# Optimization experiments

Measured on AMD Instinct MI355X. Metric: run time of the kernel, lower is better.

## Reference

```python
import jax, jax.numpy as jnp
import numpy as np

L, D, H, FF = 24, 512, 16, 2048   # n_layer, hidden_dim, heads, mlp hidden
XLEN, YLEN = 1024, 1024
EPS = 1e-5


def setup_inputs() -> dict:
    key = jax.random.key(0)
    ks = jax.random.split(key, 6)
    S = XLEN + YLEN
    s = 0.02
    return {
        "x": jax.random.normal(ks[0], (1, S, D), jnp.float32),
        "qkv_w": jax.random.normal(ks[1], (L, 3 * D, D), jnp.float32) * s,
        "qkv_b": jnp.zeros((L, 3 * D), jnp.float32),
        "out_w": jax.random.normal(ks[2], (L, D, D), jnp.float32) * s,
        "out_b": jnp.zeros((L, D), jnp.float32),
        "w1": jax.random.normal(ks[3], (L, FF, D), jnp.float32) * s,
        "b1": jnp.zeros((L, FF), jnp.float32),
        "w2": jax.random.normal(ks[4], (L, D, FF), jnp.float32) * s,
        "b2": jnp.zeros((L, D), jnp.float32),
        "norm_w1": jnp.ones((L, D), jnp.float32),
        "norm_b1": jnp.zeros((L, D), jnp.float32),
        "norm_w2": jnp.ones((L, D), jnp.float32),
        "norm_b2": jnp.zeros((L, D), jnp.float32),
        "x_len": XLEN,
        "y_len": YLEN,
    }


def _layer_norm(h, w, b):
    m = h.mean(-1, keepdims=True)
    v = ((h - m) ** 2).mean(-1, keepdims=True)
    return (h - m) * jax.lax.rsqrt(v + EPS) * w + b


def _build_mask(x_len, y_len):
    # text rows: attend to all text, never to audio; audio rows: causal over audio, full over text
    top = jnp.concatenate([jnp.zeros((x_len, x_len), bool), jnp.ones((x_len, y_len), bool)], axis=1)
    bot = jnp.concatenate([jnp.zeros((y_len, x_len), bool), jnp.triu(jnp.ones((y_len, y_len), bool), 1)], axis=1)
    bm = jnp.concatenate([top, bot], axis=0)
    # canonical_mask: bool -> additive float with -100000 at masked positions
    return jnp.where(bm, jnp.float32(-100000.0), jnp.float32(0.0))


def reference(x, qkv_w, qkv_b, out_w, out_b, w1, b1, w2, b2, norm_w1, norm_b1, norm_w2, norm_b2, x_len, y_len):
    B, S, _ = x.shape
    hd = D // H
    scale = 1.0 / np.sqrt(hd)
    mask = _build_mask(x_len, y_len)  # [S, S]

    def layer(h, p):
        qw, qb, ow, ob, W1, B1, W2, B2, nw1, nb1, nw2, nb2 = p
        qkv = h @ qw.T + qb                                   # [B,S,3D]
        q, k, v = jnp.split(qkv, 3, axis=-1)
        q = q.reshape(B, S, H, hd).transpose(0, 2, 1, 3)      # [B,H,S,hd]
        k = k.reshape(B, S, H, hd).transpose(0, 2, 1, 3)
        v = v.reshape(B, S, H, hd).transpose(0, 2, 1, 3)
        att = jax.nn.softmax(jnp.einsum('bhqd,bhkd->bhqk', q, k) * scale + mask, axis=-1)
        o = jnp.einsum('bhqk,bhkd->bhqd', att, v).transpose(0, 2, 1, 3).reshape(B, S, D)
        o = o @ ow.T + ob
        h = _layer_norm(h + o, nw1, nb1)
        m = jax.nn.relu(h @ W1.T + B1) @ W2.T + B2            # T2SMLP
        h = _layer_norm(h + m, nw2, nb2)
        return h, None

    params = (qkv_w, qkv_b, out_w, out_b, w1, b1, w2, b2, norm_w1, norm_b1, norm_w2, norm_b2)
    x, _ = jax.lax.scan(layer, x, params)
    return x
```

## Files before the change

kernel.cpp:

```cpp
#include <hip/hip_runtime.h>
#include <cstddef>

#define S_LEN 2048
#define XLEN_C 1024
#define DMODEL 512
#define NHEAD 16
#define HDIM 32
#define FFDIM 2048
#define NLAYER 24
#define TD3 1536

typedef __attribute__((ext_vector_type(4))) float f32x4;
typedef __attribute__((ext_vector_type(8))) short short8;

__device__ __forceinline__ void split2(float x, unsigned short& h, unsigned short& l) {
  unsigned u = __float_as_uint(x);
  unsigned r = u + 0x7FFFu + ((u >> 16) & 1u);
  h = (unsigned short)(r >> 16);
  float hf = __uint_as_float((unsigned)h << 16);
  float lo = x - hf;
  unsigned u2 = __float_as_uint(lo);
  unsigned r2 = u2 + 0x7FFFu + ((u2 >> 16) & 1u);
  l = (unsigned short)(r2 >> 16);
}

template<int WMF, bool RELU, bool SPLIT_OUT, bool PRESPLIT_B>
__global__ __launch_bounds__(256) void gemm_mfma(const unsigned short* __restrict__ Ahg,
                                                 const unsigned short* __restrict__ Alg,
                                                 const float* __restrict__ Bg,
                                                 const unsigned short* __restrict__ Bhg,
                                                 const unsigned short* __restrict__ Blg,
                                                 const float* __restrict__ bias,
                                                 float* __restrict__ Cf,
                                                 unsigned short* __restrict__ Ch,
                                                 unsigned short* __restrict__ Cl,
                                                 int N, int K) {
  constexpr int BM = 32 * WMF;
  __shared__ __align__(16) unsigned short Ahs[BM][40];
  __shared__ __align__(16) unsigned short Als[BM][40];
  __shared__ __align__(16) unsigned short Bhs[64][40];
  __shared__ __align__(16) unsigned short Bls[64][40];

  const int tid  = threadIdx.x;
  const int m0   = blockIdx.y * BM;
  const int n0   = blockIdx.x << 6;
  const int w    = tid >> 6;
  const int lane = tid & 63;
  const int wm   = (w >> 1) * (16 * WMF);
  const int wn   = (w & 1) << 5;
  const int fr   = lane & 15;
  const int fq   = lane >> 4;

  const int br = tid >> 2, bc = (tid & 3) << 3;

  f32x4 acc[WMF][2];
  #pragma unroll
  for (int i = 0; i < WMF; ++i)
    #pragma unroll
    for (int j = 0; j < 2; ++j)
      acc[i][j] = (f32x4){0.f, 0.f, 0.f, 0.f};

  for (int k0 = 0; k0 < K; k0 += 32) {
    short8 bh, bl;
    if (PRESPLIT_B) {
      bh = *(const short8*)&Bhg[(size_t)(n0 + br) * K + k0 + bc];
      bl = *(const short8*)&Blg[(size_t)(n0 + br) * K + k0 + bc];
    } else {
      float4 b0 = *(const float4*)&Bg[(size_t)(n0 + br) * K + k0 + bc];
      float4 b1 = *(const float4*)&Bg[(size_t)(n0 + br) * K + k0 + bc + 4];
      const float bf[8] = {b0.x, b0.y, b0.z, b0.w, b1.x, b1.y, b1.z, b1.w};
      #pragma unroll
      for (int i = 0; i < 8; ++i) {
        unsigned short h, lo; split2(bf[i], h, lo);
        bh[i] = (short)h; bl[i] = (short)lo;
      }
    }
    short8 a_h[(BM * 4) / 256], a_l[(BM * 4) / 256];
    #pragma unroll
    for (int it = 0; it < (BM * 4) / 256; ++it) {
      const int c = tid + (it << 8);
      const int arow = c >> 2, acol = (c & 3) << 3;
      a_h[it] = *(const short8*)&Ahg[(size_t)(m0 + arow) * K + k0 + acol];
      a_l[it] = *(const short8*)&Alg[(size_t)(m0 + arow) * K + k0 + acol];
    }
    __syncthreads();
    #pragma unroll
    for (int it = 0; it < (BM * 4) / 256; ++it) {
      const int c = tid + (it << 8);
      const int arow = c >> 2, acol = (c & 3) << 3;
      *(short8*)&Ahs[arow][acol] = a_h[it];
      *(short8*)&Als[arow][acol] = a_l[it];
    }
    *(short8*)&Bhs[br][bc] = bh;
    *(short8*)&Bls[br][bc] = bl;
    __syncthreads();

    short8 fah[WMF], fal[WMF], fbh[2], fbl[2];
    #pragma unroll
    for (int fm = 0; fm < WMF; ++fm) {
      fah[fm] = *(const short8*)&Ahs[wm + (fm << 4) + fr][fq << 3];
      fal[fm] = *(const short8*)&Als[wm + (fm << 4) + fr][fq << 3];
    }
    #pragma unroll
    for (int fn = 0; fn < 2; ++fn) {
      fbh[fn] = *(const short8*)&Bhs[wn + (fn << 4) + fr][fq << 3];
      fbl[fn] = *(const short8*)&Bls[wn + (fn << 4) + fr][fq << 3];
    }
    #pragma unroll
    for (int fm = 0; fm < WMF; ++fm)
      #pragma unroll
      for (int fn = 0; fn < 2; ++fn) {
        acc[fm][fn] = __builtin_amdgcn_mfma_f32_16x16x32_bf16(fah[fm], fbh[fn], acc[fm][fn], 0, 0, 0);
        acc[fm][fn] = __builtin_amdgcn_mfma_f32_16x16x32_bf16(fah[fm], fbl[fn], acc[fm][fn], 0, 0, 0);
        acc[fm][fn] = __builtin_amdgcn_mfma_f32_16x16x32_bf16(fal[fm], fbh[fn], acc[fm][fn], 0, 0, 0);
      }
  }

  #pragma unroll
  for (int fn = 0; fn < 2; ++fn) {
    const int col = n0 + wn + (fn << 4) + fr;
    const float bb = bias[col];
    #pragma unroll
    for (int fm = 0; fm < WMF; ++fm) {
      const int rbase = m0 + wm + (fm << 4) + (fq << 2);
      #pragma unroll
      for (int i = 0; i < 4; ++i) {
        float v = acc[fm][fn][i] + bb;
        if (RELU) v = fmaxf(v, 0.f);
        const size_t idx = (size_t)(rbase + i) * N + col;
        if (SPLIT_OUT) {
          unsigned short h, lo; split2(v, h, lo);
          Ch[idx] = h; Cl[idx] = lo;
        } else {
          Cf[idx] = v;
        }
      }
    }
  }
}

__global__ __launch_bounds__(256) void transpose_v(const unsigned short* __restrict__ qh,
                                                   const unsigned short* __restrict__ ql,
                                                   unsigned short* __restrict__ vth,
                                                   unsigned short* __restrict__ vtl) {
  const int hh  = blockIdx.x;
  const int t0  = blockIdx.y << 6;
  const int tid = threadIdx.x;
  __shared__ unsigned short Th[64][40];
  __shared__ unsigned short Tl[64][40];
  const int lseq = tid >> 2, dg = (tid & 3) << 3;
  const size_t src = (size_t)(t0 + lseq) * TD3 + 2 * DMODEL + (hh << 5) + dg;
  *(short8*)&Th[lseq][dg] = *(const short8*)&qh[src];
  *(short8*)&Tl[lseq][dg] = *(const short8*)&ql[src];
  __syncthreads();
  const int d = tid >> 3, sg = (tid & 7) << 3;
  short8 oh, ol;
  #pragma unroll
  for (int j = 0; j < 8; ++j) { oh[j] = (short)Th[sg + j][d]; ol[j] = (short)Tl[sg + j][d]; }
  const size_t dst = ((size_t)(hh << 5) + d) * S_LEN + t0 + sg;
  *(short8*)&vth[dst] = oh;
  *(short8*)&vtl[dst] = ol;
}

__global__ __launch_bounds__(256) void attn_mfma(const unsigned short* __restrict__ qh_g,
                                                 const unsigned short* __restrict__ ql_g,
                                                 const unsigned short* __restrict__ vth_g,
                                                 const unsigned short* __restrict__ vtl_g,
                                                 unsigned short* __restrict__ oh_g,
                                                 unsigned short* __restrict__ ol_g) {
  const int hh  = blockIdx.x;
  const int q0  = blockIdx.y << 6;
  const int tid = threadIdx.x;
  const int w   = tid >> 6;
  const int lane = tid & 63;
  const int fr = lane & 15;
  const int fq = lane >> 4;
  constexpr float SCL2 = 0.17677669529663687f * 1.44269504088896341f;

  __shared__ __align__(16) unsigned short Kh[64][40];
  __shared__ __align__(16) unsigned short Kl[64][40];
  __shared__ __align__(16) unsigned short Vth[32][72];
  __shared__ __align__(16) unsigned short Vtl[32][72];
  __shared__ __align__(16) unsigned short Ph[4][16][72];
  __shared__ __align__(16) unsigned short Pl[4][16][72];

  const int qrow = q0 + (w << 4) + fr;
  const short8 fQh = *(const short8*)&qh_g[(size_t)qrow * TD3 + hh * HDIM + (fq << 3)];
  const short8 fQl = *(const short8*)&ql_g[(size_t)qrow * TD3 + hh * HDIM + (fq << 3)];

  float m = -3.0e38f, l = 0.f;
  f32x4 accO[2];
  accO[0] = (f32x4){0.f, 0.f, 0.f, 0.f};
  accO[1] = (f32x4){0.f, 0.f, 0.f, 0.f};

  const int kend   = (q0 < XLEN_C) ? XLEN_C : (q0 + 64);
  const int ntiles = kend >> 6;

  const int krow = tid >> 2, kcol = (tid & 3) << 3;
  const int vd = tid >> 3, vseg = tid & 7;

  for (int t = 0; t < ntiles; ++t) {
    const int c0 = t << 6;
    __syncthreads();
    *(short8*)&Kh[krow][kcol] =
        *(const short8*)&qh_g[(size_t)(c0 + krow) * TD3 + DMODEL + hh * HDIM + kcol];
    *(short8*)&Kl[krow][kcol] =
        *(const short8*)&ql_g[(size_t)(c0 + krow) * TD3 + DMODEL + hh * HDIM + kcol];
    const size_t vsrc = ((size_t)(hh << 5) + vd) * S_LEN + c0 + (vseg << 3);
    *(short8*)&Vth[vd][vseg << 3] = *(const short8*)&vth_g[vsrc];
    *(short8*)&Vtl[vd][vseg << 3] = *(const short8*)&vtl_g[vsrc];
    __syncthreads();

    f32x4 s4[4];
    #pragma unroll
    for (int sub = 0; sub < 4; ++sub) {
      s4[sub] = (f32x4){0.f, 0.f, 0.f, 0.f};
      const short8 kh = *(const short8*)&Kh[(sub << 4) + fr][fq << 3];
      const short8 kl = *(const short8*)&Kl[(sub << 4) + fr][fq << 3];
      s4[sub] = __builtin_amdgcn_mfma_f32_16x16x32_bf16(kh, fQh, s4[sub], 0, 0, 0);
      s4[sub] = __builtin_amdgcn_mfma_f32_16x16x32_bf16(kh, fQl, s4[sub], 0, 0, 0);
      s4[sub] = __builtin_amdgcn_mfma_f32_16x16x32_bf16(kl, fQh, s4[sub], 0, 0, 0);
    }

    float sv[16];
    float tmax = -3.0e38f;
    #pragma unroll
    for (int sub = 0; sub < 4; ++sub)
      #pragma unroll
      for (int i = 0; i < 4; ++i) {
        const int k = c0 + (sub << 4) + (fq << 2) + i;
        const bool ok = (k < XLEN_C) | (k <= qrow);
        const float val = ok ? s4[sub][i] * SCL2 : -3.0e38f;
        sv[(sub << 2) + i] = val;
        tmax = fmaxf(tmax, val);
      }
    tmax = fmaxf(tmax, __shfl_xor(tmax, 16));
    tmax = fmaxf(tmax, __shfl_xor(tmax, 32));
    const float mnew  = fmaxf(m, tmax);
    const float alpha = exp2f(m - mnew);
    m = mnew;
    float psum = 0.f;
    unsigned short p_h[16], p_l[16];
    #pragma unroll
    for (int idx = 0; idx < 16; ++idx) {
      const float p = exp2f(sv[idx] - mnew);
      psum += p;
      split2(p, p_h[idx], p_l[idx]);
    }
    psum += __shfl_xor(psum, 16);
    psum += __shfl_xor(psum, 32);
    l = l * alpha + psum;

    #pragma unroll
    for (int sub = 0; sub < 4; ++sub) {
      ushort4 uh, ul;
      uh.x = p_h[(sub << 2) + 0]; uh.y = p_h[(sub << 2) + 1];
      uh.z = p_h[(sub << 2) + 2]; uh.w = p_h[(sub << 2) + 3];
      ul.x = p_l[(sub << 2) + 0]; ul.y = p_l[(sub << 2) + 1];
      ul.z = p_l[(sub << 2) + 2]; ul.w = p_l[(sub << 2) + 3];
      *(ushort4*)&Ph[w][fr][(sub << 4) + (fq << 2)] = uh;
      *(ushort4*)&Pl[w][fr][(sub << 4) + (fq << 2)] = ul;
    }

    const float a0 = __shfl(alpha, (fq << 2) + 0);
    const float a1 = __shfl(alpha, (fq << 2) + 1);
    const float a2 = __shfl(alpha, (fq << 2) + 2);
    const float a3 = __shfl(alpha, (fq << 2) + 3);
    #pragma unroll
    for (int df = 0; df < 2; ++df) {
      accO[df][0] *= a0; accO[df][1] *= a1;
      accO[df][2] *= a2; accO[df][3] *= a3;
    }

    #pragma unroll
    for (int kh2 = 0; kh2 < 2; ++kh2) {
      const short8 pah = *(const short8*)&Ph[w][fr][(kh2 << 5) + (fq << 3)];
      const short8 pal = *(const short8*)&Pl[w][fr][(kh2 << 5) + (fq << 3)];
      #pragma unroll
      for (int df = 0; df < 2; ++df) {
        const short8 vbh = *(const short8*)&Vth[(df << 4) + fr][(kh2 << 5) + (fq << 3)];
        const short8 vbl = *(const short8*)&Vtl[(df << 4) + fr][(kh2 << 5) + (fq << 3)];
        accO[df] = __builtin_amdgcn_mfma_f32_16x16x32_bf16(pah, vbh, accO[df], 0, 0, 0);
        accO[df] = __builtin_amdgcn_mfma_f32_16x16x32_bf16(pal, vbh, accO[df], 0, 0, 0);
        accO[df] = __builtin_amdgcn_mfma_f32_16x16x32_bf16(pah, vbl, accO[df], 0, 0, 0);
      }
    }
  }

  const float linv = 1.f / l;
  const float l0 = __shfl(linv, (fq << 2) + 0);
  const float l1 = __shfl(linv, (fq << 2) + 1);
  const float l2v = __shfl(linv, (fq << 2) + 2);
  const float l3 = __shfl(linv, (fq << 2) + 3);
  #pragma unroll
  for (int df = 0; df < 2; ++df) {
    const int col = hh * HDIM + (df << 4) + fr;
    const float vals[4] = {accO[df][0] * l0, accO[df][1] * l1,
                           accO[df][2] * l2v, accO[df][3] * l3};
    #pragma unroll
    for (int i = 0; i < 4; ++i) {
      const int row = q0 + (w << 4) + (fq << 2) + i;
      unsigned short h, lo; split2(vals[i], h, lo);
      oh_g[(size_t)row * DMODEL + col] = h;
      ol_g[(size_t)row * DMODEL + col] = lo;
    }
  }
}

__global__ __launch_bounds__(256) void add_layernorm(const float* __restrict__ h,
                                                     const float* __restrict__ r,
                                                     const float* __restrict__ w,
                                                     const float* __restrict__ b,
                                                     float* __restrict__ out,
                                                     unsigned short* __restrict__ oh,
                                                     unsigned short* __restrict__ ol) {
  const int row = blockIdx.x;
  const int tid = threadIdx.x;
  const float2 hv = *(const float2*)&h[(size_t)row * DMODEL + tid * 2];
  const float2 rv = *(const float2*)&r[(size_t)row * DMODEL + tid * 2];
  const float a0 = hv.x + rv.x, a1 = hv.y + rv.y;
  float s = a0 + a1, ss = a0 * a0 + a1 * a1;
  #pragma unroll
  for (int off = 32; off; off >>= 1) {
    s  += __shfl_xor(s, off);
    ss += __shfl_xor(ss, off);
  }
  __shared__ float sb[4], ssb[4];
  const int wid = tid >> 6;
  if ((tid & 63) == 0) { sb[wid] = s; ssb[wid] = ss; }
  __syncthreads();
  s  = sb[0] + sb[1] + sb[2] + sb[3];
  ss = ssb[0] + ssb[1] + ssb[2] + ssb[3];
  const float mean = s * (1.f / DMODEL);
  const float var  = ss * (1.f / DMODEL) - mean * mean;
  const float rs   = rsqrtf(var + 1e-5f);
  const float2 wv = *(const float2*)&w[tid * 2];
  const float2 bv = *(const float2*)&b[tid * 2];
  const float o0 = (a0 - mean) * rs * wv.x + bv.x;
  const float o1 = (a1 - mean) * rs * wv.y + bv.y;
  float2 o; o.x = o0; o.y = o1;
  *(float2*)&out[(size_t)row * DMODEL + tid * 2] = o;
  unsigned short h0, l0, h1, l1;
  split2(o0, h0, l0); split2(o1, h1, l1);
  ushort2 uh; uh.x = h0; uh.y = h1;
  ushort2 ul; ul.x = l0; ul.y = l1;
  *(ushort2*)&oh[(size_t)row * DMODEL + tid * 2] = uh;
  *(ushort2*)&ol[(size_t)row * DMODEL + tid * 2] = ul;
}

__global__ __launch_bounds__(256) void split_w(const float* __restrict__ src,
                                               unsigned short* __restrict__ h,
                                               unsigned short* __restrict__ l) {
  const int i = blockIdx.x * 256 + threadIdx.x;
  const float4 v = *(const float4*)&src[(size_t)i * 4];
  const float vf[4] = {v.x, v.y, v.z, v.w};
  ushort4 uh, ul;
  unsigned short hh, ll;
  split2(vf[0], hh, ll); uh.x = hh; ul.x = ll;
  split2(vf[1], hh, ll); uh.y = hh; ul.y = ll;
  split2(vf[2], hh, ll); uh.z = hh; ul.z = ll;
  split2(vf[3], hh, ll); uh.w = hh; ul.w = ll;
  *(ushort4*)&h[(size_t)i * 4] = uh;
  *(ushort4*)&l[(size_t)i * 4] = ul;
}

__global__ __launch_bounds__(256) void split_init(const float* __restrict__ x,
                                                  float* __restrict__ f,
                                                  unsigned short* __restrict__ h,
                                                  unsigned short* __restrict__ l,
                                                  int n4) {
  const int i = blockIdx.x * 256 + threadIdx.x;
  if (i >= n4) return;
  const float4 v = *(const float4*)&x[(size_t)i * 4];
  *(float4*)&f[(size_t)i * 4] = v;
  const float vf[4] = {v.x, v.y, v.z, v.w};
  ushort4 uh, ul;
  unsigned short hh, ll;
  split2(vf[0], hh, ll); uh.x = hh; ul.x = ll;
  split2(vf[1], hh, ll); uh.y = hh; ul.y = ll;
  split2(vf[2], hh, ll); uh.z = hh; ul.z = ll;
  split2(vf[3], hh, ll); uh.w = hh; ul.w = ll;
  *(ushort4*)&h[(size_t)i * 4] = uh;
  *(ushort4*)&l[(size_t)i * 4] = ul;
}

extern "C" void kernel_launch(void* const* d_in, const int* in_sizes, int n_in,
                              void* d_out, int out_size, void* d_ws, size_t ws_size,
                              hipStream_t stream) {
  const float* x     = (const float*)d_in[0];
  const float* qkv_w = (const float*)d_in[1];
  const float* qkv_b = (const float*)d_in[2];
  const float* out_w = (const float*)d_in[3];
  const float* out_b = (const float*)d_in[4];
  const float* w1    = (const float*)d_in[5];
  const float* b1    = (const float*)d_in[6];
  const float* w2    = (const float*)d_in[7];
  const float* b2    = (const float*)d_in[8];
  const float* nw1   = (const float*)d_in[9];
  const float* nb1   = (const float*)d_in[10];
  const float* nw2   = (const float*)d_in[11];
  const float* nb2   = (const float*)d_in[12];

  char* p = (char*)d_ws;
  float* Hc = (float*)p;                     p += (size_t)S_LEN * DMODEL * 4;
  unsigned short* Hh = (unsigned short*)p;   p += (size_t)S_LEN * DMODEL * 2;
  unsigned short* Hl = (unsigned short*)p;   p += (size_t)S_LEN * DMODEL * 2;
  unsigned short* qkvh = (unsigned short*)p; p += (size_t)S_LEN * TD3 * 2;
  unsigned short* qkvl = (unsigned short*)p; p += (size_t)S_LEN * TD3 * 2;
  unsigned short* oath = (unsigned short*)p; p += (size_t)S_LEN * DMODEL * 2;
  unsigned short* oatl = (unsigned short*)p; p += (size_t)S_LEN * DMODEL * 2;
  float* opr = (float*)p;                    p += (size_t)S_LEN * DMODEL * 4;
  unsigned short* midh = (unsigned short*)p; p += (size_t)S_LEN * FFDIM * 2;
  unsigned short* midl = (unsigned short*)p; p += (size_t)S_LEN * FFDIM * 2;
  unsigned short* vth = (unsigned short*)p;  p += (size_t)S_LEN * DMODEL * 2;
  unsigned short* vtl = (unsigned short*)p;  p += (size_t)S_LEN * DMODEL * 2;
  unsigned short* qkvWh = (unsigned short*)p; p += (size_t)NLAYER * TD3 * DMODEL * 2;
  unsigned short* qkvWl = (unsigned short*)p; p += (size_t)NLAYER * TD3 * DMODEL * 2;
  unsigned short* outWh = (unsigned short*)p; p += (size_t)NLAYER * DMODEL * DMODEL * 2;
  unsigned short* outWl = (unsigned short*)p; p += (size_t)NLAYER * DMODEL * DMODEL * 2;
  unsigned short* w1h = (unsigned short*)p;   p += (size_t)NLAYER * FFDIM * DMODEL * 2;
  unsigned short* w1l = (unsigned short*)p;   p += (size_t)NLAYER * FFDIM * DMODEL * 2;
  unsigned short* w2h = (unsigned short*)p;   p += (size_t)NLAYER * DMODEL * FFDIM * 2;
  unsigned short* w2l = (unsigned short*)p;   p += (size_t)NLAYER * DMODEL * FFDIM * 2;
  const size_t need = (size_t)(p - (char*)d_ws);
  const bool presplit = ws_size >= need;

  split_init<<<(S_LEN * DMODEL / 4 + 255) / 256, 256, 0, stream>>>(
      x, Hc, Hh, Hl, S_LEN * DMODEL / 4);

  if (presplit) {
    split_w<<<NLAYER * TD3 * DMODEL / 1024, 256, 0, stream>>>(qkv_w, qkvWh, qkvWl);
    split_w<<<NLAYER * DMODEL * DMODEL / 1024, 256, 0, stream>>>(out_w, outWh, outWl);
    split_w<<<NLAYER * FFDIM * DMODEL / 1024, 256, 0, stream>>>(w1, w1h, w1l);
    split_w<<<NLAYER * DMODEL * FFDIM / 1024, 256, 0, stream>>>(w2, w2h, w2l);
  }

  for (int l = 0; l < NLAYER; ++l) {
    const float* qw = qkv_w + (size_t)l * TD3 * DMODEL;
    const float* qb = qkv_b + (size_t)l * TD3;
    const float* ow = out_w + (size_t)l * DMODEL * DMODEL;
    const float* ob = out_b + (size_t)l * DMODEL;
    const float* W1 = w1 + (size_t)l * FFDIM * DMODEL;
    const float* B1 = b1 + (size_t)l * FFDIM;
    const float* W2 = w2 + (size_t)l * DMODEL * FFDIM;
    const float* B2 = b2 + (size_t)l * DMODEL;

    if (presplit) {
      const unsigned short* qwh = qkvWh + (size_t)l * TD3 * DMODEL;
      const unsigned short* qwl = qkvWl + (size_t)l * TD3 * DMODEL;
      const unsigned short* owh = outWh + (size_t)l * DMODEL * DMODEL;
      const unsigned short* owl = outWl + (size_t)l * DMODEL * DMODEL;
      const unsigned short* W1h = w1h + (size_t)l * FFDIM * DMODEL;
      const unsigned short* W1l = w1l + (size_t)l * FFDIM * DMODEL;
      const unsigned short* W2h = w2h + (size_t)l * DMODEL * FFDIM;
      const unsigned short* W2l = w2l + (size_t)l * DMODEL * FFDIM;

      gemm_mfma<4, false, true, true><<<dim3(TD3 / 64, S_LEN / 128), 256, 0, stream>>>(
          Hh, Hl, nullptr, qwh, qwl, qb, nullptr, qkvh, qkvl, TD3, DMODEL);
      transpose_v<<<dim3(NHEAD, S_LEN / 64), 256, 0, stream>>>(qkvh, qkvl, vth, vtl);
      attn_mfma<<<dim3(NHEAD, S_LEN / 64), 256, 0, stream>>>(qkvh, qkvl, vth, vtl, oath, oatl);
      gemm_mfma<2, false, false, true><<<dim3(DMODEL / 64, S_LEN / 64), 256, 0, stream>>>(
          oath, oatl, nullptr, owh, owl, ob, opr, nullptr, nullptr, DMODEL, DMODEL);
      add_layernorm<<<S_LEN, 256, 0, stream>>>(
          Hc, opr, nw1 + (size_t)l * DMODEL, nb1 + (size_t)l * DMODEL, Hc, Hh, Hl);
      gemm_mfma<4, true, true, true><<<dim3(FFDIM / 64, S_LEN / 128), 256, 0, stream>>>(
          Hh, Hl, nullptr, W1h, W1l, B1, nullptr, midh, midl, FFDIM, DMODEL);
      gemm_mfma<2, false, false, true><<<dim3(DMODEL / 64, S_LEN / 64), 256, 0, stream>>>(
          midh, midl, nullptr, W2h, W2l, B2, opr, nullptr, nullptr, DMODEL, FFDIM);
      add_layernorm<<<S_LEN, 256, 0, stream>>>(
          Hc, opr, nw2 + (size_t)l * DMODEL, nb2 + (size_t)l * DMODEL, Hc, Hh, Hl);
    } else {
      gemm_mfma<4, false, true, false><<<dim3(TD3 / 64, S_LEN / 128), 256, 0, stream>>>(
          Hh, Hl, qw, nullptr, nullptr, qb, nullptr, qkvh, qkvl, TD3, DMODEL);
      transpose_v<<<dim3(NHEAD, S_LEN / 64), 256, 0, stream>>>(qkvh, qkvl, vth, vtl);
      attn_mfma<<<dim3(NHEAD, S_LEN / 64), 256, 0, stream>>>(qkvh, qkvl, vth, vtl, oath, oatl);
      gemm_mfma<2, false, false, false><<<dim3(DMODEL / 64, S_LEN / 64), 256, 0, stream>>>(
          oath, oatl, ow, nullptr, nullptr, ob, opr, nullptr, nullptr, DMODEL, DMODEL);
      add_layernorm<<<S_LEN, 256, 0, stream>>>(
          Hc, opr, nw1 + (size_t)l * DMODEL, nb1 + (size_t)l * DMODEL, Hc, Hh, Hl);
      gemm_mfma<4, true, true, false><<<dim3(FFDIM / 64, S_LEN / 128), 256, 0, stream>>>(
          Hh, Hl, W1, nullptr, nullptr, B1, nullptr, midh, midl, FFDIM, DMODEL);
      gemm_mfma<2, false, false, false><<<dim3(DMODEL / 64, S_LEN / 64), 256, 0, stream>>>(
          midh, midl, W2, nullptr, nullptr, B2, opr, nullptr, nullptr, DMODEL, FFDIM);
      add_layernorm<<<S_LEN, 256, 0, stream>>>(
          Hc, opr, nw2 + (size_t)l * DMODEL, nb2 + (size_t)l * DMODEL, Hc, Hh, Hl);
    }
  }

  hipMemcpyAsync(d_out, Hc, sizeof(float) * S_LEN * DMODEL,
                 hipMemcpyDeviceToDevice, stream);
}
```

Measured before the change: 5.287 ms.

## Split attention KV range into two chunks with a log-sum-exp combine kernel

Replaces the single-pass attention kernel with a split-K variant. Each (head, query tile) is processed by two blocks over halves of the key range, which write unnormalized partial outputs plus running max and sum to workspace. A separate combine kernel merges the two halves and emits the bf16 hi/lo split output. This doubles the grid from 512 to 1024 blocks and halves the longest per-block causal loop, which should improve occupancy and load balance on a GPU with many CUs. The cost is an extra launch and extra fp32 round-trip traffic through global memory.

```diff
diff --git a/kernel.cpp b/kernel.cpp
--- a/kernel.cpp
+++ b/kernel.cpp
@@ -9,6 +9,7 @@
 #define FFDIM 2048
 #define NLAYER 24
 #define TD3 1536
+#define NQT 32
 
 typedef __attribute__((ext_vector_type(4))) float f32x4;
 typedef __attribute__((ext_vector_type(8))) short short8;
@@ -162,14 +163,17 @@
   *(short8*)&vtl[dst] = ol;
 }
 
-__global__ __launch_bounds__(256) void attn_mfma(const unsigned short* __restrict__ qh_g,
-                                                 const unsigned short* __restrict__ ql_g,
-                                                 const unsigned short* __restrict__ vth_g,
-                                                 const unsigned short* __restrict__ vtl_g,
-                                                 unsigned short* __restrict__ oh_g,
-                                                 unsigned short* __restrict__ ol_g) {
+__global__ __launch_bounds__(256) void attn_sk(const unsigned short* __restrict__ qh_g,
+                                               const unsigned short* __restrict__ ql_g,
+                                               const unsigned short* __restrict__ vth_g,
+                                               const unsigned short* __restrict__ vtl_g,
+                                               float* __restrict__ pO,
+                                               float* __restrict__ pM,
+                                               float* __restrict__ pL) {
   const int hh  = blockIdx.x;
-  const int q0  = blockIdx.y << 6;
+  const int qt  = blockIdx.y;
+  const int ck  = blockIdx.z;
+  const int q0  = qt << 6;
   const int tid = threadIdx.x;
   const int w   = tid >> 6;
   const int lane = tid & 63;
@@ -193,13 +197,15 @@
   accO[0] = (f32x4){0.f, 0.f, 0.f, 0.f};
   accO[1] = (f32x4){0.f, 0.f, 0.f, 0.f};
 
-  const int kend   = (q0 < XLEN_C) ? XLEN_C : (q0 + 64);
-  const int ntiles = kend >> 6;
+  const int nt_total = (qt < 16) ? 16 : (qt + 1);
+  const int half     = nt_total >> 1;
+  const int t_begin  = ck ? half : 0;
+  const int t_end    = ck ? nt_total : half;
 
   const int krow = tid >> 2, kcol = (tid & 3) << 3;
   const int vd = tid >> 3, vseg = tid & 7;
 
-  for (int t = 0; t < ntiles; ++t) {
+  for (int t = t_begin; t < t_end; ++t) {
     const int c0 = t << 6;
     __syncthreads();
     *(short8*)&Kh[krow][kcol] =
@@ -287,24 +293,46 @@
     }
   }
 
-  const float linv = 1.f / l;
-  const float l0 = __shfl(linv, (fq << 2) + 0);
-  const float l1 = __shfl(linv, (fq << 2) + 1);
-  const float l2v = __shfl(linv, (fq << 2) + 2);
-  const float l3 = __shfl(linv, (fq << 2) + 3);
+  const int pidx = (((hh << 5) + qt) << 1) + ck;
+  float* po = pO + (size_t)pidx * (64 * 32);
   #pragma unroll
-  for (int df = 0; df < 2; ++df) {
-    const int col = hh * HDIM + (df << 4) + fr;
-    const float vals[4] = {accO[df][0] * l0, accO[df][1] * l1,
-                           accO[df][2] * l2v, accO[df][3] * l3};
-    #pragma unroll
-    for (int i = 0; i < 4; ++i) {
-      const int row = q0 + (w << 4) + (fq << 2) + i;
-      unsigned short h, lo; split2(vals[i], h, lo);
-      oh_g[(size_t)row * DMODEL + col] = h;
-      ol_g[(size_t)row * DMODEL + col] = lo;
-    }
-  }
+  for (int df = 0; df < 2; ++df)
+    #pragma unroll
+    for (int i = 0; i < 4; ++i)
+      po[(size_t)((w << 4) + (fq << 2) + i) * 32 + (df << 4) + fr] = accO[df][i];
+  if (fq == 0) {
+    pM[pidx * 64 + (w << 4) + fr] = m;
+    pL[pidx * 64 + (w << 4) + fr] = l;
+  }
+}
+
+__global__ __launch_bounds__(256) void attn_combine(const float* __restrict__ pO,
+                                                    const float* __restrict__ pM,
+                                                    const float* __restrict__ pL,
+                                                    unsigned short* __restrict__ oh_g,
+                                                    unsigned short* __restrict__ ol_g) {
+  const int hh = blockIdx.x, qt = blockIdx.y;
+  const int tid = threadIdx.x;
+  const int row = tid >> 2;
+  const int cg  = (tid & 3) << 3;
+  const int b0  = (((hh << 5) + qt) << 1);
+  const float m0 = pM[b0 * 64 + row], m1 = pM[(b0 + 1) * 64 + row];
+  const float l0 = pL[b0 * 64 + row], l1 = pL[(b0 + 1) * 64 + row];
+  const float M  = fmaxf(m0, m1);
+  const float w0 = exp2f(m0 - M), w1 = exp2f(m1 - M);
+  const float inv = 1.f / (w0 * l0 + w1 * l1);
+  const float* o0 = pO + (size_t)b0 * 2048 + row * 32 + cg;
+  const float* o1 = pO + (size_t)(b0 + 1) * 2048 + row * 32 + cg;
+  short8 hs, ls;
+  #pragma unroll
+  for (int j = 0; j < 8; ++j) {
+    const float v = (w0 * o0[j] + w1 * o1[j]) * inv;
+    unsigned short h, lo; split2(v, h, lo);
+    hs[j] = (short)h; ls[j] = (short)lo;
+  }
+  const size_t dst = (size_t)((qt << 6) + row) * DMODEL + (hh << 5) + cg;
+  *(short8*)&oh_g[dst] = hs;
+  *(short8*)&ol_g[dst] = ls;
 }
 
 __global__ __launch_bounds__(256) void add_layernorm(const float* __restrict__ h,
@@ -414,6 +442,9 @@
   unsigned short* midl = (unsigned short*)p; p += (size_t)S_LEN * FFDIM * 2;
   unsigned short* vth = (unsigned short*)p;  p += (size_t)S_LEN * DMODEL * 2;
   unsigned short* vtl = (unsigned short*)p;  p += (size_t)S_LEN * DMODEL * 2;
+  float* pO = (float*)p;                     p += (size_t)NHEAD * NQT * 2 * 64 * 32 * 4;
+  float* pM = (float*)p;                     p += (size_t)NHEAD * NQT * 2 * 64 * 4;
+  float* pL = (float*)p;                     p += (size_t)NHEAD * NQT * 2 * 64 * 4;
   unsigned short* qkvWh = (unsigned short*)p; p += (size_t)NLAYER * TD3 * DMODEL * 2;
   unsigned short* qkvWl = (unsigned short*)p; p += (size_t)NLAYER * TD3 * DMODEL * 2;
   unsigned short* outWh = (unsigned short*)p; p += (size_t)NLAYER * DMODEL * DMODEL * 2;
@@ -458,7 +489,8 @@
       gemm_mfma<4, false, true, true><<<dim3(TD3 / 64, S_LEN / 128), 256, 0, stream>>>(
           Hh, Hl, nullptr, qwh, qwl, qb, nullptr, qkvh, qkvl, TD3, DMODEL);
       transpose_v<<<dim3(NHEAD, S_LEN / 64), 256, 0, stream>>>(qkvh, qkvl, vth, vtl);
-      attn_mfma<<<dim3(NHEAD, S_LEN / 64), 256, 0, stream>>>(qkvh, qkvl, vth, vtl, oath, oatl);
+      attn_sk<<<dim3(NHEAD, NQT, 2), 256, 0, stream>>>(qkvh, qkvl, vth, vtl, pO, pM, pL);
+      attn_combine<<<dim3(NHEAD, NQT), 256, 0, stream>>>(pO, pM, pL, oath, oatl);
       gemm_mfma<2, false, false, true><<<dim3(DMODEL / 64, S_LEN / 64), 256, 0, stream>>>(
           oath, oatl, nullptr, owh, owl, ob, opr, nullptr, nullptr, DMODEL, DMODEL);
       add_layernorm<<<S_LEN, 256, 0, stream>>>(
@@ -473,7 +505,8 @@
       gemm_mfma<4, false, true, false><<<dim3(TD3 / 64, S_LEN / 128), 256, 0, stream>>>(
           Hh, Hl, qw, nullptr, nullptr, qb, nullptr, qkvh, qkvl, TD3, DMODEL);
       transpose_v<<<dim3(NHEAD, S_LEN / 64), 256, 0, stream>>>(qkvh, qkvl, vth, vtl);
-      attn_mfma<<<dim3(NHEAD, S_LEN / 64), 256, 0, stream>>>(qkvh, qkvl, vth, vtl, oath, oatl);
+      attn_sk<<<dim3(NHEAD, NQT, 2), 256, 0, stream>>>(qkvh, qkvl, vth, vtl, pO, pM, pL);
+      attn_combine<<<dim3(NHEAD, NQT), 256, 0, stream>>>(pO, pM, pL, oath, oatl);
       gemm_mfma<2, false, false, false><<<dim3(DMODEL / 64, S_LEN / 64), 256, 0, stream>>>(
           oath, oatl, ow, nullptr, nullptr, ob, opr, nullptr, nullptr, DMODEL, DMODEL);
       add_layernorm<<<S_LEN, 256, 0, stream>>>(
```

After: 4.675 ms. 1.13x faster.
